# Performance work log

Hardware: AMD Instinct MI355X
Metric: run time of the kernel (lower is better)

Reference implementation:

```python
import jax, jax.numpy as jnp
import numpy as np

B, S, HID = 2, 1024, 2048
NH, NKV, HD = 16, 4, 128
SCALE = 1.0 / np.sqrt(HD)
ROPE_BASE = 10000.0
EPS = 1e-6


def setup_inputs() -> dict:
    key = jax.random.key(0)
    ks = jax.random.split(key, 5)
    std = 0.02
    return {
        "hidden_states": jax.random.normal(ks[0], (B, S, HID), jnp.float32),
        "Wq": jax.random.normal(ks[1], (NH * HD, HID), jnp.float32) * std,
        "Wk": jax.random.normal(ks[2], (NKV * HD, HID), jnp.float32) * std,
        "Wv": jax.random.normal(ks[3], (NKV * HD, HID), jnp.float32) * std,
        "Wo": jax.random.normal(ks[4], (HID, HID), jnp.float32) * std,
        "q_norm_w": jnp.ones((HD,), jnp.float32),
        "k_norm_w": jnp.ones((HD,), jnp.float32),
    }


def _rope(x):
    # x: [B, H, S, D]; half-split rotary
    d2 = HD // 2
    inv_freq = 1.0 / (ROPE_BASE ** (jnp.arange(0, HD, 2, dtype=jnp.float32) / HD))
    ang = jnp.arange(S, dtype=jnp.float32)[:, None] * inv_freq[None, :]  # [S, d2]
    cos, sin = jnp.cos(ang), jnp.sin(ang)
    x1, x2 = x[..., :d2], x[..., d2:]
    return jnp.concatenate([x1 * cos - x2 * sin, x1 * sin + x2 * cos], axis=-1)


def _rms(x, w):
    var = jnp.mean(jnp.square(x), axis=-1, keepdims=True)
    return x * jax.lax.rsqrt(var + EPS) * w


def reference(hidden_states, Wq, Wk, Wv, Wo, q_norm_w, k_norm_w):
    b, s, _ = hidden_states.shape
    # projections (no bias)
    q = (hidden_states @ Wq.T).reshape(b, s, NH, HD).transpose(0, 2, 1, 3)
    k = (hidden_states @ Wk.T).reshape(b, s, NKV, HD).transpose(0, 2, 1, 3)
    v = (hidden_states @ Wv.T).reshape(b, s, NKV, HD).transpose(0, 2, 1, 3)
    # RoPE then per-head-dim RMS qk-norm (shared params across heads)
    q, k = _rope(q), _rope(k)
    q, k = _rms(q, q_norm_w), _rms(k, k_norm_w)
    # GQA: repeat kv heads
    groups = NH // NKV
    k = jnp.repeat(k, groups, axis=1)
    v = jnp.repeat(v, groups, axis=1)
    # stick-breaking attention, strictly causal (attend_current=False), no normalize
    logits = jnp.einsum("bhid,bhjd->bhij", q, k) * SCALE  # [B,H,S,S]
    log_p = jax.nn.log_sigmoid(logits)
    log_om = jax.nn.log_sigmoid(-logits)  # log(1 - p)
    i = jnp.arange(s)
    mask = i[None, :] < i[:, None]  # j < i
    masked_om = jnp.where(mask, log_om, 0.0)
    # cum[i,j] = sum_{j < k < i} log(1-p[i,k]) : exclusive reversed cumsum
    cum = jnp.flip(jnp.cumsum(jnp.flip(masked_om, -1), -1), -1) - masked_om
    att = jnp.where(mask, jnp.exp(log_p + cum), 0.0)
    o = jnp.einsum("bhij,bhjd->bhid", att, v)
    o = o.transpose(0, 2, 1, 3).reshape(b, s, NH * HD)
    return o @ Wo.T
```

## Files before the change

kernel.cpp:

```cpp
#include <hip/hip_runtime.h>
#include <math.h>

#define B_    2
#define S_    1024
#define HID_  2048
#define NH_   16
#define NKV_  4
#define HD_   128
#define GROUPS (NH_ / NKV_)
#define SCALE_ 0.08838834764831845f

typedef _Float16 f16x8 __attribute__((ext_vector_type(8)));
typedef _Float16 f16x4 __attribute__((ext_vector_type(4)));
typedef float    f32x4 __attribute__((ext_vector_type(4)));

__device__ __forceinline__ void async_copy16(const void* g, void* l) {
    __builtin_amdgcn_global_load_lds(
        (const __attribute__((address_space(1))) void*)g,
        (__attribute__((address_space(3))) void*)l, 16, 0, 0);
}

__device__ __forceinline__ int dpp_swap1(int x) {
    return __builtin_amdgcn_update_dpp(0, x, 0xB1, 0xF, 0xF, true);
}

__global__ __launch_bounds__(256) void cast5_f16(
    const float4* __restrict__ s0, ushort4* __restrict__ d0, int n0,
    const float4* __restrict__ s1, ushort4* __restrict__ d1, int n1,
    const float4* __restrict__ s2, ushort4* __restrict__ d2, int n2,
    const float4* __restrict__ s3, ushort4* __restrict__ d3, int n3,
    const float4* __restrict__ s4, ushort4* __restrict__ d4, int n4)
{
    int i = blockIdx.x * 256 + threadIdx.x;
    const float4* s; ushort4* d; int idx;
    if (i < n0)                          { s = s0; d = d0; idx = i; }
    else if (i < n0 + n1)                { s = s1; d = d1; idx = i - n0; }
    else if (i < n0 + n1 + n2)           { s = s2; d = d2; idx = i - n0 - n1; }
    else if (i < n0 + n1 + n2 + n3)      { s = s3; d = d3; idx = i - n0 - n1 - n2; }
    else if (i < n0 + n1 + n2 + n3 + n4) { s = s4; d = d4; idx = i - n0 - n1 - n2 - n3; }
    else return;
    float4 v = s[idx];
    _Float16 a = (_Float16)v.x, b = (_Float16)v.y,
             c = (_Float16)v.z, e = (_Float16)v.w;
    ushort4 o;
    o.x = *(unsigned short*)&a; o.y = *(unsigned short*)&b;
    o.z = *(unsigned short*)&c; o.w = *(unsigned short*)&e;
    d[idx] = o;
}

__global__ __launch_bounds__(256) void qkv_gemm(
    const _Float16* __restrict__ A,
    const _Float16* __restrict__ Wq,
    const _Float16* __restrict__ Wk,
    const _Float16* __restrict__ Wv,
    _Float16* __restrict__ Qp,
    _Float16* __restrict__ Kp,
    _Float16* __restrict__ Vp)
{
    __shared__ __align__(16) _Float16 As[128][32];
    __shared__ __align__(16) _Float16 Ws[128][32];

    const int tid  = threadIdx.x;
    const int lane = tid & 63, wave = tid >> 6;
    const int wr = (wave >> 1) * 64, wc = (wave & 1) * 64;
    const int bm = blockIdx.y * 128;
    const int bt = blockIdx.x;
    const int z  = blockIdx.z;
    const int kbase = z * (HID_ / 2);

    const _Float16* Wsel;
    _Float16* Csel;
    int nrow0, heads;
    if (bt < 16)      { Wsel = Wq; Csel = Qp + (size_t)z * 4194304; nrow0 = bt * 128;        heads = NH_;  }
    else if (bt < 20) { Wsel = Wk; Csel = Kp + (size_t)z * 1048576; nrow0 = (bt - 16) * 128; heads = NKV_; }
    else              { Wsel = Wv; Csel = Vp + (size_t)z * 1048576; nrow0 = (bt - 20) * 128; heads = NKV_; }

    const int srow = 32 * wave + (lane >> 2);
    const int scol = (lane & 3) * 8;
    const _Float16* Ag = A    + (size_t)(bm + srow)    * HID_ + kbase + scol;
    const _Float16* Wg = Wsel + (size_t)(nrow0 + srow) * HID_ + kbase + scol;
    _Float16* lA = &As[32 * wave][0];
    _Float16* lW = &Ws[32 * wave][0];

    f32x4 acc[4][4];
    const f32x4 fz = {0.f, 0.f, 0.f, 0.f};
#pragma unroll
    for (int i = 0; i < 4; i++)
#pragma unroll
        for (int j = 0; j < 4; j++) acc[i][j] = fz;

    const int ml = lane & 15, kg = lane >> 4;

    for (int k0 = 0; k0 < HID_ / 2; k0 += 32) {
        __syncthreads();
        async_copy16(Ag + k0, lA);
        async_copy16(Ag + k0 + (size_t)16 * HID_, lA + 16 * 32);
        async_copy16(Wg + k0, lW);
        async_copy16(Wg + k0 + (size_t)16 * HID_, lW + 16 * 32);
        __syncthreads();

        f16x8 a[4], b[4];
#pragma unroll
        for (int mi = 0; mi < 4; mi++)
            a[mi] = *(const f16x8*)&As[wr + mi * 16 + ml][kg * 8];
#pragma unroll
        for (int ni = 0; ni < 4; ni++)
            b[ni] = *(const f16x8*)&Ws[wc + ni * 16 + ml][kg * 8];
#pragma unroll
        for (int mi = 0; mi < 4; mi++)
#pragma unroll
            for (int ni = 0; ni < 4; ni++)
                acc[mi][ni] = __builtin_amdgcn_mfma_f32_16x16x32_f16(
                    a[mi], b[ni], acc[mi][ni], 0, 0, 0);
    }

#pragma unroll
    for (int mi = 0; mi < 4; mi++) {
#pragma unroll
        for (int ni = 0; ni < 4; ni++) {
#pragma unroll
            for (int r = 0; r < 4; r++) {
                int m = bm + wr + mi * 16 + kg * 4 + r;
                int n = nrow0 + wc + ni * 16 + ml;
                int hh = n >> 7, d = n & 127;
                int b_ = m >> 10, s = m & 1023;
                size_t idx = (((size_t)(b_ * heads + hh)) * S_ + s) * HD_ + d;
                Csel[idx] = (_Float16)acc[mi][ni][r];
            }
        }
    }
}

__global__ __launch_bounds__(256) void out_gemm(
    const _Float16* __restrict__ A,
    const _Float16* __restrict__ W,
    _Float16* __restrict__ Op)
{
    __shared__ __align__(16) _Float16 As[128][32];
    __shared__ __align__(16) _Float16 Ws[128][32];

    const int tid  = threadIdx.x;
    const int lane = tid & 63, wave = tid >> 6;
    const int wr = (wave >> 1) * 64, wc = (wave & 1) * 64;
    const int bm = blockIdx.y * 128, bn = blockIdx.x * 128;
    const int z  = blockIdx.z;
    const int kbase = z * (HID_ / 2);
    _Float16* Cp = Op + (size_t)z * 4194304;

    const int srow = 32 * wave + (lane >> 2);
    const int scol = (lane & 3) * 8;
    const _Float16* Ag = A + (size_t)(bm + srow) * HID_ + kbase + scol;
    const _Float16* Wg = W + (size_t)(bn + srow) * HID_ + kbase + scol;
    _Float16* lA = &As[32 * wave][0];
    _Float16* lW = &Ws[32 * wave][0];

    f32x4 acc[4][4];
    const f32x4 fz = {0.f, 0.f, 0.f, 0.f};
#pragma unroll
    for (int i = 0; i < 4; i++)
#pragma unroll
        for (int j = 0; j < 4; j++) acc[i][j] = fz;

    const int ml = lane & 15, kg = lane >> 4;

    for (int k0 = 0; k0 < HID_ / 2; k0 += 32) {
        __syncthreads();
        async_copy16(Ag + k0, lA);
        async_copy16(Ag + k0 + (size_t)16 * HID_, lA + 16 * 32);
        async_copy16(Wg + k0, lW);
        async_copy16(Wg + k0 + (size_t)16 * HID_, lW + 16 * 32);
        __syncthreads();

        f16x8 a[4], b[4];
#pragma unroll
        for (int mi = 0; mi < 4; mi++)
            a[mi] = *(const f16x8*)&As[wr + mi * 16 + ml][kg * 8];
#pragma unroll
        for (int ni = 0; ni < 4; ni++)
            b[ni] = *(const f16x8*)&Ws[wc + ni * 16 + ml][kg * 8];
#pragma unroll
        for (int mi = 0; mi < 4; mi++)
#pragma unroll
            for (int ni = 0; ni < 4; ni++)
                acc[mi][ni] = __builtin_amdgcn_mfma_f32_16x16x32_f16(
                    a[mi], b[ni], acc[mi][ni], 0, 0, 0);
    }

#pragma unroll
    for (int mi = 0; mi < 4; mi++)
#pragma unroll
        for (int ni = 0; ni < 4; ni++)
#pragma unroll
            for (int r = 0; r < 4; r++) {
                int m = bm + wr + mi * 16 + kg * 4 + r;
                int n = bn + wc + ni * 16 + ml;
                Cp[(size_t)m * HID_ + n] = (_Float16)acc[mi][ni][r];
            }
}

__global__ __launch_bounds__(256) void reduce_out(
    const _Float16* __restrict__ Op, float* __restrict__ out)
{
    int i = (blockIdx.x * 256 + threadIdx.x) * 4;
    f16x4 a = *(const f16x4*)(Op + i);
    f16x4 b = *(const f16x4*)(Op + 4194304 + i);
    float4 o;
    o.x = (float)a[0] + (float)b[0];
    o.y = (float)a[1] + (float)b[1];
    o.z = (float)a[2] + (float)b[2];
    o.w = (float)a[3] + (float)b[3];
    *(float4*)(out + i) = o;
}

__global__ __launch_bounds__(256) void rope_rms_v(
    const _Float16* __restrict__ Qp, const _Float16* __restrict__ Kp,
    const _Float16* __restrict__ Vp,
    const float* __restrict__ qw, const float* __restrict__ kw,
    _Float16* __restrict__ Qout, _Float16* __restrict__ Kout,
    _Float16* __restrict__ Vout)
{
    int row = blockIdx.x * 4 + (threadIdx.x >> 6);
    int lane = threadIdx.x & 63;

    if (row >= 40960) {
        int lrow = row - 40960;
        size_t off = (size_t)lrow * HD_ + lane * 2;
        float a0 = (float)Vp[off]     + (float)Vp[1048576 + off];
        float a1 = (float)Vp[off + 1] + (float)Vp[1048576 + off + 1];
        _Float16* q = Vout + (size_t)lrow * HD_;
        q[lane * 2]     = (_Float16)a0;
        q[lane * 2 + 1] = (_Float16)a1;
        return;
    }

    bool isQ = row < 32768;
    int lrow = isQ ? row : row - 32768;
    const _Float16* p0 = isQ ? Qp : Kp;
    size_t psz = isQ ? 4194304 : 1048576;
    _Float16* q = (isQ ? Qout : Kout) + (size_t)lrow * HD_;
    const float* w = isQ ? qw : kw;
    int s = row & (S_ - 1);

    size_t base = (size_t)lrow * HD_;
    float x1 = (float)p0[base + lane]      + (float)p0[psz + base + lane];
    float x2 = (float)p0[base + lane + 64] + (float)p0[psz + base + lane + 64];

    float invf = exp2f(-(float)lane * 0.2076205059304601f);
    float ang = (float)s * invf;
    float c, sn;
    sincosf(ang, &sn, &c);

    float y1 = x1 * c - x2 * sn;
    float y2 = x1 * sn + x2 * c;

    float ss = y1 * y1 + y2 * y2;
#pragma unroll
    for (int off = 32; off > 0; off >>= 1) ss += __shfl_xor(ss, off);

    float scl = rsqrtf(ss * (1.0f / 128.0f) + 1e-6f);
    q[lane]      = (_Float16)(y1 * scl * w[lane]);
    q[lane + 64] = (_Float16)(y2 * scl * w[lane + 64]);
}

#define QK_STR 136
#define VT_STR 72
#define SS_STR 68
#define AT_STR 72

__global__ __launch_bounds__(512) void stick_attn(
    const _Float16* __restrict__ Q, const _Float16* __restrict__ K,
    const _Float16* __restrict__ V, _Float16* __restrict__ AO)
{
    __shared__ __align__(16) _Float16 Qs[64][QK_STR];
    __shared__ __align__(16) _Float16 Ks[64][QK_STR];
    __shared__ __align__(16) _Float16 Vt[128][VT_STR];
    __shared__ __align__(16) float    Ss[64][SS_STR];
    __shared__ __align__(16) _Float16 atts[64][AT_STR];
    __shared__ float paccs[64];

    const int bid = blockIdx.x;
    const int slot = bid & 255, phase = bid >> 8;
    const int hb = slot >> 3, iw = slot & 7;
    const int b = hb >> 4, h = hb & 15;
    const int qb = phase ? iw : 15 - iw;

    const int kvh = h / GROUPS;
    const int tid = threadIdx.x;
    const int lane = tid & 63, wave = tid >> 6;
    const int qw = wave >> 1;
    const int kh = wave & 1;
    const int ml = lane & 15, quad = lane >> 4;

    const _Float16* Kbase = K + ((size_t)(b * NKV_ + kvh) * S_) * HD_;
    const _Float16* Vbase = V + ((size_t)(b * NKV_ + kvh) * S_) * HD_;

    const f32x4 fz = {0.f, 0.f, 0.f, 0.f};

    const int qi0 = qb * 64;
    const _Float16* Qbase = Q + ((size_t)(b * NH_ + h) * S_ + qi0) * HD_;

    const int kr = tid >> 4, kc = (tid & 15) * 8;
    const _Float16* Vrow = Vbase + (size_t)lane * HD_ + wave * 16;

    f16x8 kA, kB, vA, vB;
    {
        const _Float16* kp = Kbase + (size_t)(qb * 64 + kr) * HD_ + kc;
        kA = *(const f16x8*)(kp);
        kB = *(const f16x8*)(kp + (size_t)32 * HD_);
        const _Float16* vp = Vrow + (size_t)(qb * 64) * HD_;
        vA = *(const f16x8*)(vp);
        vB = *(const f16x8*)(vp + 8);
    }

    for (int idx = tid; idx < 64 * 16; idx += 512) {
        int r = idx >> 4, c8 = (idx & 15) * 8;
        *(f16x8*)&Qs[r][c8] = *(const f16x8*)(Qbase + r * HD_ + c8);
    }
    if (tid < 64) paccs[tid] = 1.f;
    __syncthreads();

    f16x8 aq[4];
#pragma unroll
    for (int ks = 0; ks < 4; ks++)
        aq[ks] = *(const f16x8*)&Qs[qw * 16 + ml][ks * 32 + quad * 8];

    f32x4 accO[4] = {fz, fz, fz, fz};

    for (int kb = qb; kb >= 0; --kb) {
        __syncthreads();

        *(f16x8*)&Ks[kr][kc]      = kA;
        *(f16x8*)&Ks[kr + 32][kc] = kB;

        {
            int4 i0 = *(int4*)&vA, i1 = *(int4*)&vB;
            int4 p0, p1;
            p0.x = dpp_swap1(i0.x); p0.y = dpp_swap1(i0.y);
            p0.z = dpp_swap1(i0.z); p0.w = dpp_swap1(i0.w);
            p1.x = dpp_swap1(i1.x); p1.y = dpp_swap1(i1.y);
            p1.z = dpp_swap1(i1.z); p1.w = dpp_swap1(i1.w);
            bool ev = !(lane & 1);
            int4 al = ev ? i0 : p1;
            int4 bh = ev ? p0 : i1;
            int r0w = wave * 16 + (ev ? 0 : 8);
            int colk = lane & ~1;
            int ac[4] = {al.x, al.y, al.z, al.w};
            int bc[4] = {bh.x, bh.y, bh.z, bh.w};
#pragma unroll
            for (int i = 0; i < 8; i++) {
                int c = i >> 1;
                unsigned pack = (i & 1)
                    ? (((unsigned)ac[c] >> 16) | ((unsigned)bc[c] & 0xffff0000u))
                    : (((unsigned)ac[c] & 0xffffu) | ((unsigned)bc[c] << 16));
                *(unsigned*)&Vt[r0w + i][colk] = pack;
            }
        }
        __syncthreads();

        if (kb > 0) {
            const _Float16* kp = Kbase + (size_t)((kb - 1) * 64 + kr) * HD_ + kc;
            kA = *(const f16x8*)(kp);
            kB = *(const f16x8*)(kp + (size_t)32 * HD_);
            const _Float16* vp = Vrow + (size_t)((kb - 1) * 64) * HD_;
            vA = *(const f16x8*)(vp);
            vB = *(const f16x8*)(vp + 8);
        }

        f32x4 accS[2] = {fz, fz};
#pragma unroll
        for (int ks = 0; ks < 4; ks++) {
#pragma unroll
            for (int ni = 0; ni < 2; ni++) {
                f16x8 bf = *(const f16x8*)
                    &Ks[kh * 32 + ni * 16 + ml][ks * 32 + quad * 8];
                accS[ni] = __builtin_amdgcn_mfma_f32_16x16x32_f16(
                    aq[ks], bf, accS[ni], 0, 0, 0);
            }
        }
#pragma unroll
        for (int ni = 0; ni < 2; ni++)
#pragma unroll
            for (int r = 0; r < 4; r++)
                Ss[qw * 16 + quad * 4 + r][kh * 32 + ni * 16 + ml] =
                    accS[ni][r] * SCALE_;
        __syncthreads();

        {
            int q = tid >> 3, seg = tid & 7;
            int qg = qi0 + q;
            int j0 = kb * 64 + seg * 8;
            float4 s0 = *(float4*)&Ss[q][seg * 8];
            float4 s1 = *(float4*)&Ss[q][seg * 8 + 4];
            float L[8] = {s0.x, s0.y, s0.z, s0.w, s1.x, s1.y, s1.z, s1.w};
            float sv[8], om[8];
#pragma unroll
            for (int i = 0; i < 8; i++) {
                float u = __expf(L[i]);
                float o = __builtin_amdgcn_rcpf(1.f + u);
                bool valid = (j0 + i < qg);
                om[i] = valid ? o : 1.f;
                sv[i] = valid ? (1.f - o) : 0.f;
            }
            float suf = 1.f, lo[8];
#pragma unroll
            for (int i = 7; i >= 0; --i) {
                lo[i] = suf; suf *= om[i];
            }
            float x = suf;
#pragma unroll
            for (int off = 1; off < 8; off <<= 1) {
                float y = __shfl_down(x, off);
                if (seg + off < 8) x *= y;
            }
            float bx = __shfl_down(x, 1);
            float base = (seg == 7) ? 1.f : bx;
            float paccq = paccs[q];
            float pb = base * paccq;
            f16x8 av;
#pragma unroll
            for (int i = 0; i < 8; i++)
                av[i] = (_Float16)(sv[i] * lo[i] * pb);
            *(f16x8*)&atts[q][seg * 8] = av;
            if (seg == 0) paccs[q] = paccq * x;
        }
        __syncthreads();

#pragma unroll
        for (int ks = 0; ks < 2; ks++) {
            f16x8 ap = *(const f16x8*)&atts[qw * 16 + ml][ks * 32 + quad * 8];
#pragma unroll
            for (int ni = 0; ni < 4; ni++) {
                f16x8 bv = *(const f16x8*)
                    &Vt[kh * 64 + ni * 16 + ml][ks * 32 + quad * 8];
                accO[ni] = __builtin_amdgcn_mfma_f32_16x16x32_f16(
                    ap, bv, accO[ni], 0, 0, 0);
            }
        }
    }

#pragma unroll
    for (int ni = 0; ni < 4; ni++) {
#pragma unroll
        for (int r = 0; r < 4; r++) {
            int qg = qi0 + qw * 16 + quad * 4 + r;
            int d = kh * 64 + ni * 16 + ml;
            AO[((size_t)(b * S_ + qg) * NH_ + h) * HD_ + d] =
                (_Float16)accO[ni][r];
        }
    }
}

extern "C" void kernel_launch(void* const* d_in, const int* in_sizes, int n_in,
                              void* d_out, int out_size, void* d_ws, size_t ws_size,
                              hipStream_t stream)
{
    const float* hs = (const float*)d_in[0];
    const float* Wq = (const float*)d_in[1];
    const float* Wk = (const float*)d_in[2];
    const float* Wv = (const float*)d_in[3];
    const float* Wo = (const float*)d_in[4];
    const float* qw = (const float*)d_in[5];
    const float* kw = (const float*)d_in[6];
    float* out = (float*)d_out;

    _Float16* Qp  = (_Float16*)d_ws;
    _Float16* Kp  = Qp + 8388608;
    _Float16* Vp  = Kp + 2097152;
    _Float16* Op  = Vp + 2097152;
    _Float16* hsh = Op + 8388608;
    _Float16* Wqh = hsh + 4194304;
    _Float16* Wkh = Wqh + 4194304;
    _Float16* Wvh = Wkh + 1048576;
    _Float16* Woh = Wvh + 1048576;
    _Float16* Qh  = Woh + 4194304;
    _Float16* Kh  = Qh + 4194304;
    _Float16* Vh  = Kh + 1048576;
    _Float16* AOh = hsh;

    dim3 blk(256);

    cast5_f16<<<14336, blk, 0, stream>>>(
        (const float4*)hs, (ushort4*)hsh, 1048576,
        (const float4*)Wq, (ushort4*)Wqh, 1048576,
        (const float4*)Wk, (ushort4*)Wkh, 262144,
        (const float4*)Wv, (ushort4*)Wvh, 262144,
        (const float4*)Wo, (ushort4*)Woh, 1048576);

    qkv_gemm<<<dim3(24, 16, 2), blk, 0, stream>>>(hsh, Wqh, Wkh, Wvh,
                                                  Qp, Kp, Vp);

    rope_rms_v<<<dim3(49152 / 4), blk, 0, stream>>>(
        Qp, Kp, Vp, qw, kw, Qh, Kh, Vh);

    stick_attn<<<dim3(512), dim3(512), 0, stream>>>(Qh, Kh, Vh, AOh);

    out_gemm<<<dim3(16, 16, 2), blk, 0, stream>>>(AOh, Woh, Op);
    reduce_out<<<4096, blk, 0, stream>>>(Op, out);
}
```

Baseline: 214.9 us.

## Fuse out-projection split-K reduction into GEMM block and raise MFMA wave priority

The output GEMM now runs both K halves inside one 512-thread block, each half on its own group of four waves. The second group's accumulators are passed through shared memory and added before the fp32 result is written directly, which removes the fp16 partial buffer and the separate reduce kernel launch. This halves the grid to 256 blocks and uses about 65KB of LDS per block, which may lower occupancy. Separately, the attention kernel raises wave priority with s_setprio around its MFMA sections so matrix work gets issued ahead of other waves.

```diff
diff --git a/kernel.cpp b/kernel.cpp
--- a/kernel.cpp
+++ b/kernel.cpp
@@ -131,28 +131,29 @@
     }
 }
 
-__global__ __launch_bounds__(256) void out_gemm(
+__global__ __launch_bounds__(512) void out_gemm(
     const _Float16* __restrict__ A,
     const _Float16* __restrict__ W,
-    _Float16* __restrict__ Op)
+    float* __restrict__ Cout)
 {
-    __shared__ __align__(16) _Float16 As[128][32];
-    __shared__ __align__(16) _Float16 Ws[128][32];
+    __shared__ __align__(16) unsigned char smem[66560];
+    _Float16 (*As)[128][32] = (_Float16 (*)[128][32])smem;
+    _Float16 (*Ws)[128][32] = (_Float16 (*)[128][32])(smem + 16384);
 
     const int tid  = threadIdx.x;
     const int lane = tid & 63, wave = tid >> 6;
-    const int wr = (wave >> 1) * 64, wc = (wave & 1) * 64;
+    const int kh = wave >> 2;
+    const int wv = wave & 3;
+    const int wr = (wv >> 1) * 64, wc = (wv & 1) * 64;
     const int bm = blockIdx.y * 128, bn = blockIdx.x * 128;
-    const int z  = blockIdx.z;
-    const int kbase = z * (HID_ / 2);
-    _Float16* Cp = Op + (size_t)z * 4194304;
-
-    const int srow = 32 * wave + (lane >> 2);
+    const int kbase = kh * (HID_ / 2);
+
+    const int srow = 32 * wv + (lane >> 2);
     const int scol = (lane & 3) * 8;
     const _Float16* Ag = A + (size_t)(bm + srow) * HID_ + kbase + scol;
     const _Float16* Wg = W + (size_t)(bn + srow) * HID_ + kbase + scol;
-    _Float16* lA = &As[32 * wave][0];
-    _Float16* lW = &Ws[32 * wave][0];
+    _Float16* lA = &As[kh][32 * wv][0];
+    _Float16* lW = &Ws[kh][32 * wv][0];
 
     f32x4 acc[4][4];
     const f32x4 fz = {0.f, 0.f, 0.f, 0.f};
@@ -174,10 +175,10 @@
         f16x8 a[4], b[4];
 #pragma unroll
         for (int mi = 0; mi < 4; mi++)
-            a[mi] = *(const f16x8*)&As[wr + mi * 16 + ml][kg * 8];
+            a[mi] = *(const f16x8*)&As[kh][wr + mi * 16 + ml][kg * 8];
 #pragma unroll
         for (int ni = 0; ni < 4; ni++)
-            b[ni] = *(const f16x8*)&Ws[wc + ni * 16 + ml][kg * 8];
+            b[ni] = *(const f16x8*)&Ws[kh][wc + ni * 16 + ml][kg * 8];
 #pragma unroll
         for (int mi = 0; mi < 4; mi++)
 #pragma unroll
@@ -186,30 +187,32 @@
                     a[mi], b[ni], acc[mi][ni], 0, 0, 0);
     }
 
-#pragma unroll
-    for (int mi = 0; mi < 4; mi++)
-#pragma unroll
-        for (int ni = 0; ni < 4; ni++)
-#pragma unroll
-            for (int r = 0; r < 4; r++) {
-                int m = bm + wr + mi * 16 + kg * 4 + r;
-                int n = bn + wc + ni * 16 + ml;
-                Cp[(size_t)m * HID_ + n] = (_Float16)acc[mi][ni][r];
-            }
-}
-
-__global__ __launch_bounds__(256) void reduce_out(
-    const _Float16* __restrict__ Op, float* __restrict__ out)
-{
-    int i = (blockIdx.x * 256 + threadIdx.x) * 4;
-    f16x4 a = *(const f16x4*)(Op + i);
-    f16x4 b = *(const f16x4*)(Op + 4194304 + i);
-    float4 o;
-    o.x = (float)a[0] + (float)b[0];
-    o.y = (float)a[1] + (float)b[1];
-    o.z = (float)a[2] + (float)b[2];
-    o.w = (float)a[3] + (float)b[3];
-    *(float4*)(out + i) = o;
+    __syncthreads();
+    float* red = (float*)smem;
+    float* rp  = red + ((size_t)(wv * 64 + lane)) * 65;
+    if (kh == 1) {
+#pragma unroll
+        for (int mi = 0; mi < 4; mi++)
+#pragma unroll
+            for (int ni = 0; ni < 4; ni++)
+#pragma unroll
+                for (int r = 0; r < 4; r++)
+                    rp[mi * 16 + ni * 4 + r] = acc[mi][ni][r];
+    }
+    __syncthreads();
+    if (kh == 0) {
+#pragma unroll
+        for (int mi = 0; mi < 4; mi++)
+#pragma unroll
+            for (int ni = 0; ni < 4; ni++)
+#pragma unroll
+                for (int r = 0; r < 4; r++) {
+                    float v = acc[mi][ni][r] + rp[mi * 16 + ni * 4 + r];
+                    int m = bm + wr + mi * 16 + kg * 4 + r;
+                    int n = bn + wc + ni * 16 + ml;
+                    Cout[(size_t)m * HID_ + n] = v;
+                }
+    }
 }
 
 __global__ __launch_bounds__(256) void rope_rms_v(
@@ -367,6 +370,7 @@
         }
 
         f32x4 accS[2] = {fz, fz};
+        __builtin_amdgcn_s_setprio(1);
 #pragma unroll
         for (int ks = 0; ks < 4; ks++) {
 #pragma unroll
@@ -377,6 +381,7 @@
                     aq[ks], bf, accS[ni], 0, 0, 0);
             }
         }
+        __builtin_amdgcn_s_setprio(0);
 #pragma unroll
         for (int ni = 0; ni < 2; ni++)
 #pragma unroll
@@ -425,6 +430,7 @@
         }
         __syncthreads();
 
+        __builtin_amdgcn_s_setprio(1);
 #pragma unroll
         for (int ks = 0; ks < 2; ks++) {
             f16x8 ap = *(const f16x8*)&atts[qw * 16 + ml][ks * 32 + quad * 8];
@@ -436,6 +442,7 @@
                     ap, bv, accO[ni], 0, 0, 0);
             }
         }
+        __builtin_amdgcn_s_setprio(0);
     }
 
 #pragma unroll
@@ -466,8 +473,7 @@
     _Float16* Qp  = (_Float16*)d_ws;
     _Float16* Kp  = Qp + 8388608;
     _Float16* Vp  = Kp + 2097152;
-    _Float16* Op  = Vp + 2097152;
-    _Float16* hsh = Op + 8388608;
+    _Float16* hsh = Vp + 2097152;
     _Float16* Wqh = hsh + 4194304;
     _Float16* Wkh = Wqh + 4194304;
     _Float16* Wvh = Wkh + 1048576;
@@ -494,6 +500,5 @@
 
     stick_attn<<<dim3(512), dim3(512), 0, stream>>>(Qh, Kh, Vh, AOh);
 
-    out_gemm<<<dim3(16, 16, 2), blk, 0, stream>>>(AOh, Woh, Op);
-    reduce_out<<<4096, blk, 0, stream>>>(Op, out);
-}
+    out_gemm<<<dim3(16, 16), dim3(512), 0, stream>>>(AOh, Woh, out);
+}
```

New measurement: 217.3 us. Within noise of the previous version (+1.1%).
